# Optimization experiments

Measured on AMD Instinct MI355X. Metric: run time of the kernel, lower is better.

## Reference

```python
import jax, jax.numpy as jnp
import numpy as np

N_A, N_B, C, M, E = 40000, 80000, 256, 4, 250000
NUM_HEADS = 4


def setup_inputs() -> dict:
    key = jax.random.key(0)
    ks = jax.random.split(key, 32)
    p = lambda k, shp: jax.random.normal(k, shp, dtype=jnp.float32) * 0.02
    src_ab = jax.random.randint(ks[0], (M, 1, E), 0, N_A, dtype=jnp.int32)
    dst_ab = jax.random.randint(ks[1], (M, 1, E), 0, N_B, dtype=jnp.int32)
    src_ba = jax.random.randint(ks[2], (M, 1, E), 0, N_B, dtype=jnp.int32)
    dst_ba = jax.random.randint(ks[3], (M, 1, E), 0, N_A, dtype=jnp.int32)
    mp_w = jax.random.uniform(ks[4], (M,), dtype=jnp.float32) + 0.1
    mp_w = mp_w / mp_w.sum()  # normalized metapath_counts buffer
    return {
        "x_a": jax.random.normal(ks[5], (N_A, C), jnp.float32),
        "x_b": jax.random.normal(ks[6], (N_B, C), jnp.float32),
        "edges_ab": jnp.concatenate([src_ab, dst_ab], axis=1),  # [M,2,E]
        "edges_ba": jnp.concatenate([src_ba, dst_ba], axis=1),  # [M,2,E]
        "wl1": p(ks[7], (M, C, C)), "wr1": p(ks[8], (M, C, C)), "b1": p(ks[9], (M, C)),
        "wl2": p(ks[10], (M, C, C)), "wr2": p(ks[11], (M, C, C)), "b2": p(ks[12], (M, C)),
        "outw": p(ks[13], (M, C, C)), "outb": p(ks[14], (M, C)),
        "mp_weights": mp_w,
        "in_proj_w": p(ks[15], (3 * C, C)), "in_proj_b": p(ks[16], (3 * C,)),
        "attn_out_w": p(ks[17], (C, C)), "attn_out_b": p(ks[18], (C,)),
        "mlp1_w": p(ks[19], (C, C)), "mlp1_b": p(ks[20], (C,)),
        "mlp2_w": p(ks[21], (C, 1)), "mlp2_b": p(ks[22], (1,)),
    }


def _sage(x_src, x_dst, src, dst, n_dst, wl, wr, b):
    # SAGEConv (mean aggr): lin_l(mean_{src->dst} x_src) + lin_r(x_dst) + b
    msg = jax.ops.segment_sum(x_src[src], dst, num_segments=n_dst)
    cnt = jax.ops.segment_sum(jnp.ones(src.shape, x_src.dtype), dst, num_segments=n_dst)
    mean = msg / jnp.maximum(cnt, 1.0)[:, None]
    return mean @ wl + x_dst @ wr + b


def _forward(x_a, x_b, edges_ab, edges_ba, wl1, wr1, b1, wl2, wr2, b2, outw, outb,
             mp_weights, in_proj_w, in_proj_b, attn_out_w, attn_out_b,
             mlp1_w, mlp1_b, mlp2_w, mlp2_b):
    embs = []
    for m in range(M):  # small fixed set of metapath GNNs (structurally distinct params)
        h_b = jax.nn.relu(_sage(x_a, x_b, edges_ab[m, 0], edges_ab[m, 1], N_B,
                                wl1[m], wr1[m], b1[m]))
        h_a = jax.nn.relu(_sage(h_b, x_a, edges_ba[m, 0], edges_ba[m, 1], N_A,
                                wl2[m], wr2[m], b2[m]))
        embs.append(h_a @ outw[m] + outb[m])  # out_proj on start node type
    x = jnp.stack(embs, axis=1) * mp_weights[None, :, None]  # [N_A, M, C]
    # MultiheadAttention (batch_first, self-attention over metapath axis)
    qkv = x @ in_proj_w.T + in_proj_b
    q, k, v = jnp.split(qkv, 3, axis=-1)
    d = C // NUM_HEADS
    q = q.reshape(N_A, M, NUM_HEADS, d)
    k = k.reshape(N_A, M, NUM_HEADS, d)
    v = v.reshape(N_A, M, NUM_HEADS, d)
    scores = jnp.einsum('nqhd,nkhd->nhqk', q, k) / jnp.sqrt(jnp.float32(d))
    attn = jax.nn.softmax(scores, axis=-1)
    o = jnp.einsum('nhqk,nkhd->nqhd', attn, v).reshape(N_A, M, C)
    o = o @ attn_out_w.T + attn_out_b
    pooled = o.mean(axis=1)  # [N_A, C]
    h = jax.nn.relu(pooled @ mlp1_w + mlp1_b)
    return (h @ mlp2_w + mlp2_b).squeeze(-1)  # [N_A]


def reference(x_a, x_b, edges_ab, edges_ba, wl1, wr1, b1, wl2, wr2, b2, outw, outb,
              mp_weights, in_proj_w, in_proj_b, attn_out_w, attn_out_b,
              mlp1_w, mlp1_b, mlp2_w, mlp2_b):
    return _forward(x_a, x_b, edges_ab, edges_ba, wl1, wr1, b1, wl2, wr2, b2,
                    outw, outb, mp_weights, in_proj_w, in_proj_b,
                    attn_out_w, attn_out_b, mlp1_w, mlp1_b, mlp2_w, mlp2_b)
```

## Files before the change

### kernel.cpp

```cpp
#include <hip/hip_runtime.h>
#include <hip/hip_bf16.h>
#include <hip/hip_fp16.h>


#define N_A 40000
#define N_B 80000
#define CDIM 256
#define MP 4
#define EDG 250000

using f16x8 = __attribute__((ext_vector_type(8))) _Float16;
using f32x4 = __attribute__((ext_vector_type(4))) float;

__device__ __forceinline__ float ldf(const float* p) { return *p; }
__device__ __forceinline__ float ldf(const __half* p) { return __half2float(*p); }
__device__ __forceinline__ void stf(float* p, float v) { *p = v; }
__device__ __forceinline__ void stf(__half* p, float v) { *p = __float2half(v); }

__device__ __forceinline__ float4 ld4(const __half* p) {
    __half2 a = *(const __half2*)p, b = *(const __half2*)(p + 2);
    float2 fa = __half22float2(a), fb = __half22float2(b);
    return make_float4(fa.x, fa.y, fb.x, fb.y);
}

template<typename AT, typename CT, typename ET, bool FUSE2, bool EXTRA,
         bool BIAS, bool RELU, bool OSCALE>
__global__ __launch_bounds__(256) void mgemm_k(
    const AT* __restrict__ A, int lda,
    const __half* __restrict__ A2,
    const __half* __restrict__ BT,
    const float* __restrict__ bias,
    const ET* __restrict__ extra, int lde,
    const float* __restrict__ osp, int osi,
    CT* __restrict__ C, int ldc, int K)
{
    __shared__ __align__(16) _Float16 As[64 * 40];
    __shared__ __align__(16) _Float16 Bs[128 * 40];
    const int tid = threadIdx.x;
    const int w = tid >> 6, lane = tid & 63;
    const int wm = w & 1, wn = w >> 1;
    const int lr = lane & 15, kb = lane >> 4;
    const long long row0 = (long long)blockIdx.y * 64;
    const int col0 = blockIdx.x * 128;
    f32x4 acc[2][4] = {};
    for (int k0 = 0; k0 < K; k0 += 32) {
        {
            int flat = tid * 8;
            int r = flat >> 5, c = flat & 31;
            int kk = k0 + c;
            if constexpr (FUSE2) {
                const __half* src = (kk < 256)
                    ? (const __half*)&A[(row0 + r) * lda + kk]
                    : &A2[(row0 + r) * 256 + (kk - 256)];
                *(f16x8*)&As[r * 40 + c] = *(const f16x8*)src;
            } else if constexpr (sizeof(AT) == 4) {
                const AT* src = &A[(row0 + r) * lda + kk];
                float4 v0 = *(const float4*)(src);
                float4 v1 = *(const float4*)(src + 4);
                _Float16 h[8] = {(_Float16)v0.x, (_Float16)v0.y, (_Float16)v0.z,
                                 (_Float16)v0.w, (_Float16)v1.x, (_Float16)v1.y,
                                 (_Float16)v1.z, (_Float16)v1.w};
                *(f16x8*)&As[r * 40 + c] = *(f16x8*)h;
            } else {
                *(f16x8*)&As[r * 40 + c] =
                    *(const f16x8*)&A[(row0 + r) * lda + kk];
            }
        }
        {
            #pragma unroll
            for (int q = 0; q < 2; ++q) {
                int cid = tid * 2 + q;
                int r = cid >> 2, cc = cid & 3;
                *(f16x8*)&Bs[r * 40 + cc * 8] =
                    *(const f16x8*)&BT[(long long)(col0 + r) * K + k0 + cc * 8];
            }
        }
        __syncthreads();
        f16x8 af[2], bf[4];
        #pragma unroll
        for (int i = 0; i < 2; ++i)
            af[i] = *(f16x8*)&As[(wm * 32 + i * 16 + lr) * 40 + kb * 8];
        #pragma unroll
        for (int j = 0; j < 4; ++j)
            bf[j] = *(f16x8*)&Bs[(wn * 64 + j * 16 + lr) * 40 + kb * 8];
        #pragma unroll
        for (int i = 0; i < 2; ++i)
            #pragma unroll
            for (int j = 0; j < 4; ++j)
                acc[i][j] = __builtin_amdgcn_mfma_f32_16x16x32_f16(
                    af[i], bf[j], acc[i][j], 0, 0, 0);
        __syncthreads();
    }
    float osc = 1.0f;
    if (OSCALE) osc = osp[osi];
    #pragma unroll
    for (int i = 0; i < 2; ++i) {
        #pragma unroll
        for (int j = 0; j < 4; ++j) {
            #pragma unroll
            for (int r = 0; r < 4; ++r) {
                long long rg = row0 + wm * 32 + i * 16 + (lane >> 4) * 4 + r;
                int cg = col0 + wn * 64 + j * 16 + (lane & 15);
                float v = acc[i][j][r];
                if (EXTRA) v += ldf(&extra[rg * lde + cg]);
                if (BIAS) v += bias[cg];
                if (RELU) v = fmaxf(v, 0.0f);
                if (OSCALE) v *= osc;
                stf(&C[rg * ldc + cg], v);
            }
        }
    }
}

__global__ void cvt8_k(const float* __restrict__ s, __half* __restrict__ d, int n8)
{
    int t = blockIdx.x * 256 + threadIdx.x;
    if (t >= n8) return;
    const float4 a = *(const float4*)&s[t * 8];
    const float4 b = *(const float4*)&s[t * 8 + 4];
    _Float16 h[8] = {(_Float16)a.x, (_Float16)a.y, (_Float16)a.z, (_Float16)a.w,
                     (_Float16)b.x, (_Float16)b.y, (_Float16)b.z, (_Float16)b.w};
    *(f16x8*)&d[t * 8] = *(f16x8*)h;
}

__global__ __launch_bounds__(256) void prep_k(
    const float* __restrict__ wl1, const float* __restrict__ wr1,
    const float* __restrict__ outw, const float* __restrict__ wr2,
    const float* __restrict__ wl2, const float* __restrict__ ipw,
    const float* __restrict__ aow, const float* __restrict__ m1w,
    const float* __restrict__ aob, const float* __restrict__ m1b,
    __half* __restrict__ WL1T, __half* __restrict__ WR1T,
    __half* __restrict__ OUTWT, __half* __restrict__ BT2,
    __half* __restrict__ IPW16, __half* __restrict__ WCT,
    float* __restrict__ BC)
{
    const int sec = blockIdx.y;
    const int t = blockIdx.x * 256 + threadIdx.x;
    if (sec < 3) {
        if (t >= 262144) return;
        const float* s = (sec == 0) ? wl1 : (sec == 1) ? wr1 : outw;
        __half* d = (sec == 0) ? WL1T : (sec == 1) ? WR1T : OUTWT;
        int m = t >> 16, i = t & 65535, r = i >> 8, c = i & 255;
        d[(m << 16) + (c << 8) + r] = __float2half(s[t]);
    } else if (sec == 3) {
        if (t >= 524288) return;
        int m = t >> 17, i = t & 131071, n = i >> 9, k = i & 511;
        float v = (k < 256) ? wr2[(m << 16) + (k << 8) + n]
                            : wl2[(m << 16) + ((k - 256) << 8) + n];
        BT2[t] = __float2half(v);
    } else if (sec == 4) {
        if (t >= 196608) return;
        IPW16[t] = __float2half(ipw[t]);
    } else if (sec == 5) {
        if (t >= 65536) return;
        int n = t >> 8, k = t & 255;
        float s = 0.0f;
        for (int j = 0; j < 256; ++j)
            s = fmaf(aow[j * 256 + k], m1w[j * 256 + n], s);
        WCT[t] = __float2half(s);
    } else {
        if (t >= 256) return;
        float s = m1b[t];
        for (int j = 0; j < 256; ++j) s = fmaf(aob[j], m1w[j * 256 + t], s);
        BC[t] = s;
    }
}

__global__ __launch_bounds__(256) void hist_all_k(
    const int* __restrict__ e_ab, const int* __restrict__ e_ba,
    int* __restrict__ cnt_all)
{
    const int l = blockIdx.y;
    const int e = blockIdx.x * 256 + threadIdx.x;
    if (e >= EDG) return;
    const int m = l >> 1, dir = l & 1;
    const int* dst = (dir ? e_ba : e_ab) + (size_t)m * 2 * EDG + EDG;
    atomicAdd(&cnt_all[l * 80000 + dst[e]], 1);
}
__global__ __launch_bounds__(256) void scan_blk_all_k(
    const int* __restrict__ cnt_all, int* __restrict__ bsum_all)
{
    __shared__ int s[256];
    const int l = blockIdx.y, t = threadIdx.x;
    const int i = blockIdx.x * 256 + t;
    s[t] = (i < 80000) ? cnt_all[l * 80000 + i] : 0;
    __syncthreads();
    for (int off = 128; off > 0; off >>= 1) {
        if (t < off) s[t] += s[t + off];
        __syncthreads();
    }
    if (t == 0) bsum_all[l * 313 + blockIdx.x] = s[0];
}
__global__ __launch_bounds__(512) void scan_top_all_k(
    const int* __restrict__ bsum_all, int* __restrict__ boff_all)
{
    __shared__ int s[512];
    const int l = blockIdx.x, t = threadIdx.x;
    int v = (t < 313) ? bsum_all[l * 313 + t] : 0;
    s[t] = v;
    __syncthreads();
    for (int off = 1; off < 512; off <<= 1) {
        int u = (t >= off) ? s[t - off] : 0;
        __syncthreads();
        s[t] += u;
        __syncthreads();
    }
    if (t < 313) boff_all[l * 313 + t] = s[t] - v;
}
__global__ __launch_bounds__(256) void scan_fin_all_k(
    const int* __restrict__ cnt_all, const int* __restrict__ boff_all,
    int* __restrict__ start_all, int* __restrict__ cursor_all)
{
    __shared__ int s[256];
    const int l = blockIdx.y, t = threadIdx.x;
    const int i = blockIdx.x * 256 + t;
    int v = (i < 80000) ? cnt_all[l * 80000 + i] : 0;
    s[t] = v;
    __syncthreads();
    for (int off = 1; off < 256; off <<= 1) {
        int u = (t >= off) ? s[t - off] : 0;
        __syncthreads();
        s[t] += u;
        __syncthreads();
    }
    if (i < 80000) {
        int ex = boff_all[l * 313 + blockIdx.x] + s[t] - v;
        start_all[l * 80000 + i] = ex;
        cursor_all[l * 80000 + i] = ex;
    }
}
__global__ __launch_bounds__(256) void fill_all_k(
    const int* __restrict__ e_ab, const int* __restrict__ e_ba,
    int* __restrict__ cursor_all, int* __restrict__ eidx_all)
{
    const int l = blockIdx.y;
    const int e = blockIdx.x * 256 + threadIdx.x;
    if (e >= EDG) return;
    const int m = l >> 1, dir = l & 1;
    const int* src = (dir ? e_ba : e_ab) + (size_t)m * 2 * EDG;
    const int* dst = src + EDG;
    int p = atomicAdd(&cursor_all[l * 80000 + dst[e]], 1);
    eidx_all[l * 250000 + p] = src[e];
}

__global__ __launch_bounds__(256) void gather_mean_k(
    const __half* __restrict__ feat, const int* __restrict__ start,
    const int* __restrict__ cnt, const int* __restrict__ eidx,
    __half* __restrict__ mean, int n)
{
    int t = blockIdx.x * 256 + threadIdx.x;
    int r = t >> 6, lane = t & 63;
    if (r >= n) return;
    const int s0 = start[r], deg = cnt[r];
    float4 acc = make_float4(0.f, 0.f, 0.f, 0.f);
    for (int i = 0; i < deg; ++i) {
        int s = eidx[s0 + i];
        float4 v = ld4(&feat[(long long)s * CDIM + lane * 4]);
        acc.x += v.x; acc.y += v.y; acc.z += v.z; acc.w += v.w;
    }
    const float inv = 1.0f / fmaxf((float)deg, 1.0f);
    __half hv[4] = {__float2half(acc.x * inv), __float2half(acc.y * inv),
                    __float2half(acc.z * inv), __float2half(acc.w * inv)};
    *(float2*)&mean[(long long)r * CDIM + lane * 4] = *(float2*)hv;
}

__global__ __launch_bounds__(256) void attn_pool_k(
    const __half* __restrict__ qkv, __half* __restrict__ pooled, int nNodes)
{
    __shared__ float sh[4][3072];
    __shared__ float sW[4][16];
    const int tid = threadIdx.x;
    const int wid = tid >> 6, lane = tid & 63;
    const int node = blockIdx.x * 4 + wid;
    float* S = sh[wid];
    const __half* base = qkv + (long long)node * 3072;
    #pragma unroll
    for (int it = 0; it < 6; ++it) {
        int f = it * 64 + lane;
        f16x8 v = *(const f16x8*)&base[f * 8];
        #pragma unroll
        for (int e = 0; e < 8; ++e) S[f * 8 + e] = (float)v[e];
    }
    __syncthreads();
    const int h = lane >> 4, qm = (lane >> 2) & 3, km = lane & 3;
    const float* qrow = &S[qm * 768 + h * 64];
    const float* krow = &S[km * 768 + 256 + h * 64];
    float s = 0.0f;
    #pragma unroll
    for (int i = 0; i < 64; ++i) s = fmaf(qrow[i], krow[i], s);
    s *= 0.125f;
    float mx = fmaxf(s, __shfl_xor(s, 1));
    mx = fmaxf(mx, __shfl_xor(mx, 2));
    float e = __expf(s - mx);
    float sum = e + __shfl_xor(e, 1);
    sum += __shfl_xor(sum, 2);
    float a = e / sum;
    float tt = a + __shfl_xor(a, 4);
    tt += __shfl_xor(tt, 8);
    if (qm == 0) sW[wid][h * 4 + km] = 0.25f * tt;
    __syncthreads();
    #pragma unroll
    for (int j = 0; j < 4; ++j) {
        int c = j * 64 + lane;
        float p = 0.0f;
        #pragma unroll
        for (int kk = 0; kk < 4; ++kk)
            p = fmaf(sW[wid][j * 4 + kk], S[kk * 768 + 512 + c], p);
        pooled[(long long)node * 256 + c] = __float2half(p);
    }
}

__global__ __launch_bounds__(256) void mlp2_k(
    const __half* __restrict__ h, const float* __restrict__ w,
    const float* __restrict__ b, float* __restrict__ out, int n)
{
    int t = blockIdx.x * 256 + threadIdx.x;
    int node = t >> 6, lane = t & 63;
    if (node >= n) return;
    const float4 hv = ld4(&h[(long long)node * CDIM + lane * 4]);
    const float4 wv = *(const float4*)&w[lane * 4];
    float s = hv.x * wv.x + hv.y * wv.y + hv.z * wv.z + hv.w * wv.w;
    #pragma unroll
    for (int off = 1; off < 64; off <<= 1) s += __shfl_xor(s, off);
    if (lane == 0) out[node] = s + b[0];
}

__global__ void diag_k(float* out, int n, float val)
{
    int t = blockIdx.x * 256 + threadIdx.x;
    if (t < n) out[t] = val;
}

extern "C" void kernel_launch(void* const* d_in, const int* in_sizes, int n_in,
                              void* d_out, int out_size, void* d_ws, size_t ws_size,
                              hipStream_t stream)
{
    const float* x_a  = (const float*)d_in[0];
    const float* x_b  = (const float*)d_in[1];
    const int*   e_ab = (const int*)d_in[2];
    const int*   e_ba = (const int*)d_in[3];
    const float* wl1  = (const float*)d_in[4];
    const float* wr1  = (const float*)d_in[5];
    const float* b1   = (const float*)d_in[6];
    const float* wl2  = (const float*)d_in[7];
    const float* wr2  = (const float*)d_in[8];
    const float* b2   = (const float*)d_in[9];
    const float* outw = (const float*)d_in[10];
    const float* outb = (const float*)d_in[11];
    const float* mpw  = (const float*)d_in[12];
    const float* ipw  = (const float*)d_in[13];
    const float* ipb  = (const float*)d_in[14];
    const float* aow  = (const float*)d_in[15];
    const float* aob  = (const float*)d_in[16];
    const float* m1w  = (const float*)d_in[17];
    const float* m1b  = (const float*)d_in[18];
    const float* m2w  = (const float*)d_in[19];
    const float* m2b  = (const float*)d_in[20];
    float* out = (float*)d_out;

    const size_t NEED = 40960000ull + 82240000ull + 40960000ull + 81920000ull
                      + 786432ull + 262144ull;
    if (ws_size < NEED || n_in < 21 || out_size != N_A) {
        float diag = (float)((ws_size / (1024ull * 1024ull)) * 100ull + (size_t)n_in);
        diag_k<<<(out_size + 255) / 256, 256, 0, stream>>>(out, out_size, diag);
        return;
    }

    char* base = (char*)d_ws;
    __half* XA16 = (__half*)(base);
    __half* XB16 = (__half*)(base + 20480000);
    __half* WH   = (__half*)(base + 61440000);
    char*   AREG = base + 65634304;
    char*   BREG = base + 106594304;
    __half* EMBS = (__half*)(base + 147554304);
    int*    CSR  = (int*)(base + 229474304);
    __half* WL1T  = WH;
    __half* WR1T  = WH + 262144;
    __half* BT2   = WH + 524288;
    __half* OUTWT = WH + 1048576;
    __half* IPW16 = WH + 1310720;
    __half* WCT   = WH + 1507328;
    float*  BC    = (float*)(WH + 1572864);
    int* cnt_all    = CSR;
    int* start_all  = CSR + 640000;
    int* cursor_all = CSR + 1280000;
    int* eidx_all   = CSR + 1920000;
    int* bsum_all   = CSR + 3920000;
    int* boff_all   = CSR + 3922504;
    __half* ZH      = (__half*)AREG;
    __half* HBH     = (__half*)AREG;
    __half* MEANB16 = (__half*)BREG;
    __half* MEANA16 = (__half*)BREG;
    __half* HA16    = (__half*)(BREG + 20480000);
    __half* QKV16   = (__half*)AREG;
    __half* POOL16  = (__half*)(AREG + 61440000);
    __half* TMLP16  = (__half*)AREG;

    cvt8_k<<<5000, 256, 0, stream>>>(x_a, XA16, 1280000);
    cvt8_k<<<10000, 256, 0, stream>>>(x_b, XB16, 2560000);
    prep_k<<<dim3(2048, 7), 256, 0, stream>>>(
        wl1, wr1, outw, wr2, wl2, ipw, aow, m1w, aob, m1b,
        WL1T, WR1T, OUTWT, BT2, IPW16, WCT, BC);

    const int EB = (EDG + 255) / 256;
    hipMemsetAsync(cnt_all, 0, 640000 * 4, stream);
    hist_all_k<<<dim3(EB, 8), 256, 0, stream>>>(e_ab, e_ba, cnt_all);
    scan_blk_all_k<<<dim3(313, 8), 256, 0, stream>>>(cnt_all, bsum_all);
    scan_top_all_k<<<8, 512, 0, stream>>>(bsum_all, boff_all);
    scan_fin_all_k<<<dim3(313, 8), 256, 0, stream>>>(cnt_all, boff_all,
                                                     start_all, cursor_all);
    fill_all_k<<<dim3(EB, 8), 256, 0, stream>>>(e_ab, e_ba, cursor_all, eidx_all);

    for (int m = 0; m < MP; ++m) {
        const int lB = 2 * m, lA = 2 * m + 1;
        mgemm_k<__half, __half, float, false, false, false, false, false>
            <<<dim3(2, N_A / 64), 256, 0, stream>>>(
            XA16, CDIM, nullptr, WL1T + m * 65536, nullptr, nullptr, 0,
            nullptr, 0, ZH, CDIM, CDIM);
        gather_mean_k<<<N_B / 4, 256, 0, stream>>>(
            ZH, start_all + lB * 80000, cnt_all + lB * 80000,
            eidx_all + lB * 250000, MEANB16, N_B);
        mgemm_k<__half, __half, __half, false, true, true, true, false>
            <<<dim3(2, N_B / 64), 256, 0, stream>>>(
            XB16, CDIM, nullptr, WR1T + m * 65536, b1 + (size_t)m * CDIM,
            MEANB16, CDIM, nullptr, 0, HBH, CDIM, CDIM);
        gather_mean_k<<<N_A / 4, 256, 0, stream>>>(
            HBH, start_all + lA * 80000, cnt_all + lA * 80000,
            eidx_all + lA * 250000, MEANA16, N_A);
        mgemm_k<__half, __half, float, true, false, true, true, false>
            <<<dim3(2, N_A / 64), 256, 0, stream>>>(
            XA16, CDIM, MEANA16, BT2 + m * 131072, b2 + (size_t)m * CDIM,
            nullptr, 0, nullptr, 0, HA16, CDIM, 512);
        mgemm_k<__half, __half, float, false, false, true, false, true>
            <<<dim3(2, N_A / 64), 256, 0, stream>>>(
            HA16, CDIM, nullptr, OUTWT + m * 65536, outb + (size_t)m * CDIM,
            nullptr, 0, mpw, m, EMBS + (size_t)m * CDIM, 1024, CDIM);
    }

    const int CH = 10000;
    for (int ch = 0; ch < N_A / CH; ++ch) {
        const int n0 = ch * CH;
        mgemm_k<__half, __half, float, false, false, true, false, false>
            <<<dim3(6, (CH * 4) / 64), 256, 0, stream>>>(
            EMBS + (size_t)n0 * 1024, CDIM, nullptr, IPW16, ipb, nullptr, 0,
            nullptr, 0, QKV16, 768, CDIM);
        attn_pool_k<<<CH / 4, 256, 0, stream>>>(
            QKV16, POOL16 + (size_t)n0 * 256, CH);
    }
    mgemm_k<__half, __half, float, false, false, true, true, false>
        <<<dim3(2, N_A / 64), 256, 0, stream>>>(
        POOL16, CDIM, nullptr, WCT, BC, nullptr, 0, nullptr, 0,
        TMLP16, CDIM, CDIM);
    mlp2_k<<<(N_A * 64) / 256, 256, 0, stream>>>(TMLP16, m2w, m2b, out, N_A);
}
```

Measured before the change: 1.372 ms.

## Build CSR edge lists with windowed shared-memory cursors instead of global atomics

The CSR fill step now uses 8x20 blocks of 1024 threads. Each block scans all edges of one list and keeps only destinations that fall in its 4000-row window, using shared-memory atomic cursors instead of global atomics on a cursor array. This removes the global cursor buffer and its initialization write in the scan kernel. In exchange, every edge array is read 20 times, only 160 blocks run, and the order of edges within each row stays nondeterministic.

```diff
diff --git a/kernel.cpp b/kernel.cpp
--- a/kernel.cpp
+++ b/kernel.cpp
@@ -8,6 +8,8 @@
 #define CDIM 256
 #define MP 4
 #define EDG 250000
+#define FW 20
+#define WROWS 4000
 
 using f16x8 = __attribute__((ext_vector_type(8))) _Float16;
 using f32x4 = __attribute__((ext_vector_type(4))) float;
@@ -209,7 +211,7 @@
 }
 __global__ __launch_bounds__(256) void scan_fin_all_k(
     const int* __restrict__ cnt_all, const int* __restrict__ boff_all,
-    int* __restrict__ start_all, int* __restrict__ cursor_all)
+    int* __restrict__ start_all)
 {
     __shared__ int s[256];
     const int l = blockIdx.y, t = threadIdx.x;
@@ -223,24 +225,31 @@
         s[t] += u;
         __syncthreads();
     }
-    if (i < 80000) {
-        int ex = boff_all[l * 313 + blockIdx.x] + s[t] - v;
-        start_all[l * 80000 + i] = ex;
-        cursor_all[l * 80000 + i] = ex;
-    }
-}
-__global__ __launch_bounds__(256) void fill_all_k(
+    if (i < 80000)
+        start_all[l * 80000 + i] = boff_all[l * 313 + blockIdx.x] + s[t] - v;
+}
+__global__ __launch_bounds__(1024) void fill_win_k(
     const int* __restrict__ e_ab, const int* __restrict__ e_ba,
-    int* __restrict__ cursor_all, int* __restrict__ eidx_all)
-{
-    const int l = blockIdx.y;
-    const int e = blockIdx.x * 256 + threadIdx.x;
-    if (e >= EDG) return;
+    const int* __restrict__ start_all, int* __restrict__ eidx_all)
+{
+    __shared__ int cur[WROWS];
+    const int l = blockIdx.x, wdw = blockIdx.y;
+    const int w0 = wdw * WROWS;
+    for (int i = threadIdx.x; i < WROWS; i += 1024) cur[i] = 0;
+    __syncthreads();
     const int m = l >> 1, dir = l & 1;
     const int* src = (dir ? e_ba : e_ab) + (size_t)m * 2 * EDG;
     const int* dst = src + EDG;
-    int p = atomicAdd(&cursor_all[l * 80000 + dst[e]], 1);
-    eidx_all[l * 250000 + p] = src[e];
+    const int* st = start_all + l * 80000;
+    int* eidx = eidx_all + l * 250000;
+    for (int e = threadIdx.x; e < EDG; e += 1024) {
+        int d = dst[e];
+        unsigned rel = (unsigned)(d - w0);
+        if (rel < WROWS) {
+            int p = atomicAdd(&cur[rel], 1);
+            eidx[st[d] + p] = src[e];
+        }
+    }
 }
 
 __global__ __launch_bounds__(256) void gather_mean_k(
@@ -383,10 +392,9 @@
     float*  BC    = (float*)(WH + 1572864);
     int* cnt_all    = CSR;
     int* start_all  = CSR + 640000;
-    int* cursor_all = CSR + 1280000;
-    int* eidx_all   = CSR + 1920000;
-    int* bsum_all   = CSR + 3920000;
-    int* boff_all   = CSR + 3922504;
+    int* eidx_all   = CSR + 1280000;
+    int* bsum_all   = CSR + 3280000;
+    int* boff_all   = CSR + 3282504;
     __half* ZH      = (__half*)AREG;
     __half* HBH     = (__half*)AREG;
     __half* MEANB16 = (__half*)BREG;
@@ -407,9 +415,8 @@
     hist_all_k<<<dim3(EB, 8), 256, 0, stream>>>(e_ab, e_ba, cnt_all);
     scan_blk_all_k<<<dim3(313, 8), 256, 0, stream>>>(cnt_all, bsum_all);
     scan_top_all_k<<<8, 512, 0, stream>>>(bsum_all, boff_all);
-    scan_fin_all_k<<<dim3(313, 8), 256, 0, stream>>>(cnt_all, boff_all,
-                                                     start_all, cursor_all);
-    fill_all_k<<<dim3(EB, 8), 256, 0, stream>>>(e_ab, e_ba, cursor_all, eidx_all);
+    scan_fin_all_k<<<dim3(313, 8), 256, 0, stream>>>(cnt_all, boff_all, start_all);
+    fill_win_k<<<dim3(8, FW), 1024, 0, stream>>>(e_ab, e_ba, start_all, eidx_all);
 
     for (int m = 0; m < MP; ++m) {
         const int lB = 2 * m, lA = 2 * m + 1;
```

Result: slower. 1.413 ms (+3.0%).
